# Performance work log

Measured on AMD Instinct MI355X. Metric: run time of the kernel, lower is better.

Reference implementation:

```python
import jax, jax.numpy as jnp
import numpy as np

D_MODEL = 256
N_HEADS = 8
HEAD_DIM = D_MODEL // N_HEADS


def setup_inputs() -> dict:
    key = jax.random.key(0)
    ks = jax.random.split(key, 10)
    B, L, D = 2, 2048, D_MODEL
    s = 1.0 / np.sqrt(D)
    inp = {
        "x": jax.random.normal(ks[0], (B, L, D), dtype=jnp.float32),
        "Wq": jax.random.normal(ks[1], (D, D), dtype=jnp.float32) * s,
        "bq": jnp.zeros((D,), jnp.float32),
        "Wk": jax.random.normal(ks[2], (D, D), dtype=jnp.float32) * s,
        "bk": jnp.zeros((D,), jnp.float32),
        "Wv": jax.random.normal(ks[3], (D, D), dtype=jnp.float32) * s,
        "bv": jnp.zeros((D,), jnp.float32),
        "u": jax.random.normal(ks[4], (N_HEADS, 1, 1), dtype=jnp.float32) * 0.1,
        "Wo": jax.random.normal(ks[5], (D, D), dtype=jnp.float32) * s,
        "bo": jnp.zeros((D,), jnp.float32),
    }
    return inp


def reference(x, Wq, bq, Wk, bk, Wv, bv, u, Wo, bo):
    B, L, D = x.shape
    H, hd = N_HEADS, HEAD_DIM

    def proj(W, b):  # torch Linear: x @ W.T + b -> [B,H,L,hd]
        return (x @ W.T + b).reshape(B, L, H, hd).transpose(0, 2, 1, 3)

    Q, K, V = proj(Wq, bq), proj(Wk, bk), proj(Wv, bv)

    scores = jnp.einsum("bhqd,bhkd->bhqk", Q, K) / np.sqrt(hd)
    attn_series = jax.nn.softmax(scores, axis=-1)  # [B,H,L,L]

    pos = jnp.arange(L, dtype=jnp.float32)
    dist = jnp.abs(pos[None, :] - pos[:, None])  # [L,L]
    # prior per head: exp(-d^2 / (2*(u^2+1e-6))), normalized over last dim
    prior = jnp.exp(-(dist[None] ** 2) / (2.0 * (u ** 2 + 1e-6)))  # [H,L,L]
    prior = prior / (prior.sum(axis=-1, keepdims=True) + 1e-6)

    discrepancy = jnp.abs(attn_series - prior[None]).mean(axis=(1, 2))  # [B,L]

    out = jnp.einsum("bhqk,bhkd->bhqd", attn_series, V)
    out = out.transpose(0, 2, 1, 3).reshape(B, L, D)
    out = out @ Wo.T + bo
    return out, discrepancy
```

## Files before the change

### kernel.cpp

```cpp
#include <hip/hip_runtime.h>
#include <hip/hip_bf16.h>
#include <math.h>

#define LSEQ 2048
#define DMODEL 256
#define NH 8
#define HD 32

typedef __attribute__((ext_vector_type(8))) short bf16x8;
typedef __attribute__((ext_vector_type(4))) float f32x4;

#define MFMA __builtin_amdgcn_mfma_f32_16x16x32_bf16

__device__ __forceinline__ short f2bf(float x) {
  __hip_bfloat16 h = __float2bfloat16(x);
  return __builtin_bit_cast(short, h);
}
__device__ __forceinline__ float bf2f(short s) {
  __hip_bfloat16 h = __builtin_bit_cast(__hip_bfloat16, s);
  return __bfloat162float(h);
}
__device__ __forceinline__ short bftrunc(float x) {
  return (short)(__builtin_bit_cast(unsigned int, x) >> 16);
}
__device__ __forceinline__ float fexp2(float x) {
#if __has_builtin(__builtin_amdgcn_exp2f)
  return __builtin_amdgcn_exp2f(x);
#else
  return __expf(x * 0.6931471805599453f);
#endif
}

__global__ __launch_bounds__(256) void aux_kernel(
    const float* __restrict__ x,
    const float* __restrict__ Wq, const float* __restrict__ Wk,
    const float* __restrict__ Wv, const float* __restrict__ Wo,
    const float* __restrict__ u,
    short* __restrict__ xh,
    short* __restrict__ Wh,
    short* __restrict__ Woh, short* __restrict__ Wol,
    float* __restrict__ Eb, float* __restrict__ Zb)
{
  __shared__ float Cs[LSEQ];
  __shared__ float part[256];
  const int tid = threadIdx.x;
  if (blockIdx.x < 1024) {
    const int i4 = (blockIdx.x * 256 + tid) * 4;
    float4 v = *(const float4*)(x + i4);
    *(short4*)(xh + i4) = make_short4(f2bf(v.x), f2bf(v.y), f2bf(v.z), f2bf(v.w));
    return;
  }
  const int bx = blockIdx.x - 1024;
  if (bx < 256) {
    const int i4 = (bx * 256 + tid) * 4;
    if (i4 < 196608) {
      int row = i4 >> 8, col = i4 & 255;
      const float* W = (row < 256) ? Wq : (row < 512) ? Wk : Wv;
      float4 v = *(const float4*)(W + (row & 255) * 256 + col);
      *(short4*)(Wh + i4) = make_short4(f2bf(v.x), f2bf(v.y), f2bf(v.z), f2bf(v.w));
    } else {
      int j = i4 - 196608;
      float4 v = *(const float4*)(Wo + j);
      short h0 = f2bf(v.x), h1 = f2bf(v.y), h2 = f2bf(v.z), h3 = f2bf(v.w);
      *(short4*)(Woh + j) = make_short4(h0, h1, h2, h3);
      *(short4*)(Wol + j) = make_short4(bftrunc(v.x - bf2f(h0)), bftrunc(v.y - bf2f(h1)),
                                        bftrunc(v.z - bf2f(h2)), bftrunc(v.w - bf2f(h3)));
    }
    return;
  }
  const int h = bx - 256;
  const float uu = u[h];
  const float den = 2.0f * (uu * uu + 1e-6f);
  float e[8]; float run = 0.f;
  const int base = tid * 8;
#pragma unroll
  for (int j = 0; j < 8; ++j) {
    float d = (float)(base + j);
    e[j] = __expf(-(d * d) / den);
    run += e[j];
  }
  part[tid] = run;
  __syncthreads();
  for (int off = 1; off < 256; off <<= 1) {
    float v = (tid >= off) ? part[tid - off] : 0.f;
    __syncthreads();
    part[tid] += v;
    __syncthreads();
  }
  float c = part[tid] - run;
#pragma unroll
  for (int j = 0; j < 8; ++j) {
    c += e[j];
    Cs[base + j] = c;
    Eb[h * LSEQ + base + j] = e[j];
  }
  __syncthreads();
  const float E0 = Cs[0];
  for (int i = tid; i < LSEQ; i += 256) {
    float s = Cs[i] + Cs[LSEQ - 1 - i] - E0;
    Zb[h * LSEQ + i] = 1.0f / (s + 1e-6f);
  }
}

__global__ __launch_bounds__(256) void qkv_gemm(
    const short* __restrict__ xh,
    const short* __restrict__ Bh,
    const float* __restrict__ bq, const float* __restrict__ bk,
    const float* __restrict__ bv,
    short* __restrict__ Qf, short* __restrict__ Kf, short* __restrict__ Vf)
{
  const int tid = threadIdx.x, w = tid >> 6, lane = tid & 63;
  const int l15 = lane & 15, q4 = lane >> 4;
  const int m0 = blockIdx.x * 64, n0 = blockIdx.y * 64;
  const int mrow = m0 + w * 16 + l15;
  f32x4 acc[4] = {{0,0,0,0},{0,0,0,0},{0,0,0,0},{0,0,0,0}};
  for (int k0 = 0; k0 < 256; k0 += 32) {
    bf16x8 ah = *(const bf16x8*)&xh[(size_t)mrow * 256 + k0 + q4 * 8];
#pragma unroll
    for (int nt = 0; nt < 4; ++nt) {
      const size_t bi = (size_t)(n0 + nt * 16 + l15) * 256 + k0 + q4 * 8;
      bf16x8 bh = *(const bf16x8*)&Bh[bi];
      acc[nt] = MFMA(ah, bh, acc[nt], 0, 0, 0);
    }
  }
  const int type = n0 >> 8;
  const int n0l = n0 & 255;
  const float* bias = (type == 0) ? bq : (type == 1) ? bk : bv;
  const float qls = 0.25503489f;
#pragma unroll
  for (int nt = 0; nt < 4; ++nt) {
    const int col = n0l + nt * 16 + l15;
    const float bvv = bias[col];
    const int hh = col >> 5, dloc = col & 31;
#pragma unroll
    for (int r = 0; r < 4; ++r) {
      const int m = m0 + w * 16 + q4 * 4 + r;
      float v = acc[nt][r] + bvv;
      const int bb = m >> 11, mm = m & 2047, rr = mm & 15;
      if (type == 2) {
        const int kt128 = mm >> 7, low7 = mm & 127;
        const int wv = (low7 >> 4) & 3, ph = low7 >> 6;
        const int c = ph * 16 + rr;
        const size_t idx =
          ((((((size_t)bb * 8 + hh) * 16 + kt128) * 4 + wv) * 2 + (dloc >> 4)) * 64
           + (c >> 3) * 16 + (dloc & 15)) * 8 + (c & 7);
        Vf[idx] = f2bf(v);
      } else if (type == 0) {
        const int qblk = mm >> 5, rg = (mm >> 4) & 1;
        const size_t idx =
          (((((size_t)bb * 8 + hh) * 64 + qblk) * 2 + rg) * 64
           + (dloc >> 3) * 16 + rr) * 8 + (dloc & 7);
        Qf[idx] = f2bf(v * qls);
      } else {
        const int g = mm >> 4;
        const size_t idx =
          ((((size_t)bb * 8 + hh) * 128 + g) * 64
           + (dloc >> 3) * 16 + rr) * 8 + (dloc & 7);
        Kf[idx] = f2bf(v);
      }
    }
  }
}

__global__ __launch_bounds__(512, 2) void attn_kernel(
    const short* __restrict__ Qf, const short* __restrict__ Kf,
    const short* __restrict__ Vf,
    const float* __restrict__ Eb, const float* __restrict__ Zb,
    short* __restrict__ Ohb, short* __restrict__ Olb,
    short* __restrict__ Dp)
{
  __shared__ short Pt[8][16][36];
  __shared__ float Elds[192];
  __shared__ float lpart[8][16];
  __shared__ float lpn[16];
  __shared__ float liz[16];

  const int tid = threadIdx.x, w = tid >> 6, lane = tid & 63;
  const int l15 = lane & 15, q4 = lane >> 4;
  const int flat = blockIdx.x + 128 * (blockIdx.y + 8 * blockIdx.z);
  const int slot = flat >> 3;
  const int g = (flat & 7) | ((slot >> 7) << 3);
  const int h = g & 7, b = g >> 3;
  const int qslot = slot & 127, q0 = qslot * 16;
  const int bh = b * NH + h;

  if (tid < 192) Elds[tid] = Eb[h * LSEQ + tid];
  if (tid < 16)  liz[tid] = Zb[h * LSEQ + q0 + tid];

  const bf16x8* Qf8 = (const bf16x8*)Qf;
  const bf16x8* Kf8 = (const bf16x8*)Kf;
  const bf16x8* Vf8 = (const bf16x8*)Vf;

  bf16x8 qh = Qf8[((size_t)bh * 128 + qslot) * 64 + lane];

  const size_t kfb = (size_t)bh * 128;
  const size_t vfb = (size_t)bh * 16;
  const int wv = w & 3, wh = w >> 2;

  unsigned int pc[8][4];
  float lac[4] = {0.f, 0.f, 0.f, 0.f};
  f32x4 oacc[2] = {{0,0,0,0},{0,0,0,0}};

#pragma unroll
  for (int it = 0; it < 8; ++it) {
    const int g16 = it * 16 + wh * 8 + wv;
    bf16x8 k0 = Kf8[(kfb + g16) * 64 + lane];
    bf16x8 k1 = Kf8[(kfb + g16 + 4) * 64 + lane];
    const int kt128 = it * 2 + wh;
    bf16x8 vb0 = Vf8[(((vfb + kt128) * 4 + wv) * 2 + 0) * 64 + lane];
    bf16x8 vb1 = Vf8[(((vfb + kt128) * 4 + wv) * 2 + 1) * 64 + lane];
    f32x4 s0 = {0.f,0.f,0.f,0.f}; s0 = MFMA(qh, k0, s0, 0, 0, 0);
    f32x4 s1 = {0.f,0.f,0.f,0.f}; s1 = MFMA(qh, k1, s1, 0, 0, 0);
    short c0[4], c1[4];
#pragma unroll
    for (int r = 0; r < 4; ++r) {
      float p0 = fexp2(s0[r]);
      float p1 = fexp2(s1[r]);
      lac[r] += p0 + p1;
      c0[r] = f2bf(p0);
      c1[r] = f2bf(p1);
      Pt[w][q4 * 4 + r][l15]      = c0[r];
      Pt[w][q4 * 4 + r][16 + l15] = c1[r];
    }
    pc[it][0] = (unsigned int)(unsigned short)c0[0] | ((unsigned int)(unsigned short)c0[1] << 16);
    pc[it][1] = (unsigned int)(unsigned short)c0[2] | ((unsigned int)(unsigned short)c0[3] << 16);
    pc[it][2] = (unsigned int)(unsigned short)c1[0] | ((unsigned int)(unsigned short)c1[1] << 16);
    pc[it][3] = (unsigned int)(unsigned short)c1[2] | ((unsigned int)(unsigned short)c1[3] << 16);
    bf16x8 pa = *(const bf16x8*)&Pt[w][l15][q4 * 8];
    oacc[0] = MFMA(pa, vb0, oacc[0], 0, 0, 0);
    oacc[1] = MFMA(pa, vb1, oacc[1], 0, 0, 0);
  }

#pragma unroll
  for (int r = 0; r < 4; ++r) {
    float v = lac[r];
    v += __shfl_xor(v, 1); v += __shfl_xor(v, 2);
    v += __shfl_xor(v, 4); v += __shfl_xor(v, 8);
    if (l15 == 0) lpart[w][q4 * 4 + r] = v;
  }
  __syncthreads();
  if (tid < 16) {
    float l = 0.f;
#pragma unroll
    for (int w8 = 0; w8 < 8; ++w8) l += lpart[w8][tid];
    lpn[tid] = 1.0f / l;
  }
  __syncthreads();

  float pn4[4], iz4[4];
#pragma unroll
  for (int r = 0; r < 4; ++r) {
    pn4[r] = lpn[q4 * 4 + r];
    iz4[r] = liz[q4 * 4 + r];
  }
  const int qrow0 = q0 + q4 * 4;

  const size_t drow = (size_t)(g * 128 + qslot) * LSEQ;
#pragma unroll
  for (int it = 0; it < 8; ++it) {
#pragma unroll
    for (int ph = 0; ph < 2; ++ph) {
      const int c0g = (it * 2 + wh) * 128 + ph * 64 + wv * 16;
      const int kg = c0g + l15;
      const int dd = c0g - q0;
      const bool near = (dd >= -96) && (dd <= 96);
      const unsigned int wlo = pc[it][ph * 2 + 0];
      const unsigned int whi = pc[it][ph * 2 + 1];
      float pr[4];
      pr[0] = __builtin_bit_cast(float, wlo << 16);
      pr[1] = __builtin_bit_cast(float, wlo & 0xffff0000u);
      pr[2] = __builtin_bit_cast(float, whi << 16);
      pr[3] = __builtin_bit_cast(float, whi & 0xffff0000u);
      float dsum = 0.f;
      if (near) {
#pragma unroll
        for (int r = 0; r < 4; ++r) {
          float p = pr[r] * pn4[r];
          int qrow = qrow0 + r;
          int dist = (qrow >= kg) ? (qrow - kg) : (kg - qrow);
          dsum += fabsf(p - Elds[dist] * iz4[r]);
        }
      } else {
        dsum = pr[0] * pn4[0] + pr[1] * pn4[1] + pr[2] * pn4[2] + pr[3] * pn4[3];
      }
      dsum += __shfl_xor(dsum, 16);
      dsum += __shfl_xor(dsum, 32);
      if (q4 == 0) Dp[drow + kg] = f2bf(dsum);
    }
  }

  __syncthreads();
  float* Ored = (float*)Pt;
#pragma unroll
  for (int dt = 0; dt < 2; ++dt) {
#pragma unroll
    for (int r = 0; r < 4; ++r)
      Ored[(w * 16 + q4 * 4 + r) * 17 + l15] = oacc[dt][r];
    __syncthreads();
    if (tid < 256) {
      const int q = tid >> 4, d = tid & 15;
      float v = 0.f;
#pragma unroll
      for (int w8 = 0; w8 < 8; ++w8) v += Ored[(w8 * 16 + q) * 17 + d];
      v *= lpn[q];
      const size_t oo = ((size_t)b * LSEQ + q0 + q) * DMODEL + h * HD + dt * 16 + d;
      short hi = f2bf(v);
      Ohb[oo] = hi;
      Olb[oo] = bftrunc(v - bf2f(hi));
    }
    __syncthreads();
  }
}

__global__ __launch_bounds__(256) void tail_kernel(
    const short* __restrict__ Ah, const short* __restrict__ Al,
    const short* __restrict__ Bh, const short* __restrict__ Bl,
    const float* __restrict__ bias, float* __restrict__ C,
    const short* __restrict__ Dp, float* __restrict__ disc)
{
  __shared__ float red[8][33];
  const int tid = threadIdx.x;
  if (blockIdx.x < 512) {
    const int w = tid >> 6, lane = tid & 63;
    const int l15 = lane & 15, q4 = lane >> 4;
    const int m0 = (blockIdx.x & 63) * 64, n0 = (blockIdx.x >> 6) * 32;
    const int mrow = m0 + w * 16 + l15;
    f32x4 acc[2] = {{0,0,0,0},{0,0,0,0}};
    for (int k0 = 0; k0 < 256; k0 += 32) {
      bf16x8 ah = *(const bf16x8*)&Ah[(size_t)mrow * 256 + k0 + q4 * 8];
      bf16x8 al = *(const bf16x8*)&Al[(size_t)mrow * 256 + k0 + q4 * 8];
#pragma unroll
      for (int nt = 0; nt < 2; ++nt) {
        const size_t bi = (size_t)(n0 + nt * 16 + l15) * 256 + k0 + q4 * 8;
        bf16x8 bh = *(const bf16x8*)&Bh[bi];
        bf16x8 bl = *(const bf16x8*)&Bl[bi];
        acc[nt] = MFMA(ah, bh, acc[nt], 0, 0, 0);
        acc[nt] = MFMA(al, bh, acc[nt], 0, 0, 0);
        acc[nt] = MFMA(ah, bl, acc[nt], 0, 0, 0);
      }
    }
#pragma unroll
    for (int nt = 0; nt < 2; ++nt) {
      const int col = n0 + nt * 16 + l15;
      const float bvv = bias[col];
#pragma unroll
      for (int r = 0; r < 4; ++r) {
        const int m = m0 + w * 16 + q4 * 4 + r;
        C[(size_t)m * 256 + col] = acc[nt][r] + bvv;
      }
    }
    return;
  }
  const int bid = blockIdx.x - 512;
  const int b = bid >> 6, kb = (bid & 63) * 32;
  const int k = kb + (tid & 31), sg = tid >> 5;
  float acc = 0.f;
  const short* base = Dp + ((size_t)b * 1024 + (size_t)sg * 128) * LSEQ + k;
#pragma unroll 4
  for (int i = 0; i < 128; ++i) acc += bf2f(base[(size_t)i * LSEQ]);
  red[sg][tid & 31] = acc;
  __syncthreads();
  if (tid < 32) {
    float v = 0.f;
#pragma unroll
    for (int s2 = 0; s2 < 8; ++s2) v += red[s2][tid];
    disc[b * LSEQ + kb + tid] = v * (1.0f / ((float)NH * (float)LSEQ));
  }
}

extern "C" void kernel_launch(void* const* d_in, const int* in_sizes, int n_in,
                              void* d_out, int out_size, void* d_ws, size_t ws_size,
                              hipStream_t stream)
{
  const float* x  = (const float*)d_in[0];
  const float* Wq = (const float*)d_in[1];
  const float* bq = (const float*)d_in[2];
  const float* Wk = (const float*)d_in[3];
  const float* bk = (const float*)d_in[4];
  const float* Wv = (const float*)d_in[5];
  const float* bv = (const float*)d_in[6];
  const float* u  = (const float*)d_in[7];
  const float* Wo = (const float*)d_in[8];
  const float* bo = (const float*)d_in[9];

  float* out  = (float*)d_out;
  float* disc = out + (size_t)2 * LSEQ * DMODEL;

  char* w8 = (char*)d_ws;
  const size_t MB = 1u << 20;
  short* Qfb = (short*)(w8);
  short* Kfb = (short*)(w8 + 2 * MB);
  short* Vfb = (short*)(w8 + 4 * MB);
  short* Ohb = (short*)(w8 + 6 * MB);
  short* Olb = (short*)(w8 + 8 * MB);
  short* Wh  = (short*)(w8 + 10 * MB);
  short* Woh = (short*)(w8 + 10 * MB + 393216);
  short* Wol = (short*)(w8 + 10 * MB + 524288);
  float* Eb  = (float*)(w8 + 11 * MB);
  float* Zb  = (float*)(w8 + 11 * MB + 65536);
  short* xh  = (short*)(w8 + 12 * MB);
  short* Dp  = (short*)(w8 + 14 * MB);

  aux_kernel<<<1288, 256, 0, stream>>>(x, Wq, Wk, Wv, Wo, u, xh, Wh, Woh, Wol, Eb, Zb);
  qkv_gemm<<<dim3(64, 12), 256, 0, stream>>>(xh, Wh, bq, bk, bv, Qfb, Kfb, Vfb);
  attn_kernel<<<dim3(128, 8, 2), 512, 0, stream>>>(Qfb, Kfb, Vfb, Eb, Zb,
                                                   Ohb, Olb, Dp);
  tail_kernel<<<640, 256, 0, stream>>>(Ohb, Olb, Woh, Wol, bo, out, Dp, disc);
}
```

Before: 172.7 us.

## Split attention key range across 16 waves and pack P with byte-permute truncation

The attention block grows from 512 to 1024 threads, so each of 16 waves handles 4 key tiles instead of 8, halving per-wave serial work and the register array holding packed probabilities. The bf16 conversion of probabilities switches from round-to-nearest to truncation, packed with a single v_perm, which cuts conversion ALU work but slightly changes numerics. Cross-wave reductions now sum 16 partials, and the launch bound asks for 8 blocks per CU, which may force heavy register limiting and extra shared memory per block.

```diff
diff --git a/kernel.cpp b/kernel.cpp
--- a/kernel.cpp
+++ b/kernel.cpp
@@ -29,6 +29,11 @@
 #else
   return __expf(x * 0.6931471805599453f);
 #endif
+}
+__device__ __forceinline__ unsigned int packtrunc(float lo, float hi) {
+  return __builtin_amdgcn_perm(__builtin_bit_cast(unsigned int, hi),
+                               __builtin_bit_cast(unsigned int, lo),
+                               0x07060302u);
 }
 
 __global__ __launch_bounds__(256) void aux_kernel(
@@ -162,16 +167,16 @@
   }
 }
 
-__global__ __launch_bounds__(512, 2) void attn_kernel(
+__global__ __launch_bounds__(1024, 8) void attn_kernel(
     const short* __restrict__ Qf, const short* __restrict__ Kf,
     const short* __restrict__ Vf,
     const float* __restrict__ Eb, const float* __restrict__ Zb,
     short* __restrict__ Ohb, short* __restrict__ Olb,
     short* __restrict__ Dp)
 {
-  __shared__ short Pt[8][16][36];
+  __shared__ short Pt[16][16][36];
   __shared__ float Elds[192];
-  __shared__ float lpart[8][16];
+  __shared__ float lpart[16][16];
   __shared__ float lpn[16];
   __shared__ float liz[16];
 
@@ -195,37 +200,35 @@
 
   const size_t kfb = (size_t)bh * 128;
   const size_t vfb = (size_t)bh * 16;
-  const int wv = w & 3, wh = w >> 2;
-
-  unsigned int pc[8][4];
+  const int wv = w & 3, wq = w >> 2;
+
+  unsigned int pc[4][4];
   float lac[4] = {0.f, 0.f, 0.f, 0.f};
   f32x4 oacc[2] = {{0,0,0,0},{0,0,0,0}};
 
 #pragma unroll
-  for (int it = 0; it < 8; ++it) {
-    const int g16 = it * 16 + wh * 8 + wv;
-    bf16x8 k0 = Kf8[(kfb + g16) * 64 + lane];
-    bf16x8 k1 = Kf8[(kfb + g16 + 4) * 64 + lane];
-    const int kt128 = it * 2 + wh;
+  for (int it = 0; it < 4; ++it) {
+    const int kt128 = wq + 4 * it;
+    const int gk = kt128 * 8 + wv;
+    bf16x8 k0 = Kf8[(kfb + gk) * 64 + lane];
+    bf16x8 k1 = Kf8[(kfb + gk + 4) * 64 + lane];
     bf16x8 vb0 = Vf8[(((vfb + kt128) * 4 + wv) * 2 + 0) * 64 + lane];
     bf16x8 vb1 = Vf8[(((vfb + kt128) * 4 + wv) * 2 + 1) * 64 + lane];
     f32x4 s0 = {0.f,0.f,0.f,0.f}; s0 = MFMA(qh, k0, s0, 0, 0, 0);
     f32x4 s1 = {0.f,0.f,0.f,0.f}; s1 = MFMA(qh, k1, s1, 0, 0, 0);
-    short c0[4], c1[4];
+    float p0[4], p1[4];
 #pragma unroll
     for (int r = 0; r < 4; ++r) {
-      float p0 = fexp2(s0[r]);
-      float p1 = fexp2(s1[r]);
-      lac[r] += p0 + p1;
-      c0[r] = f2bf(p0);
-      c1[r] = f2bf(p1);
-      Pt[w][q4 * 4 + r][l15]      = c0[r];
-      Pt[w][q4 * 4 + r][16 + l15] = c1[r];
-    }
-    pc[it][0] = (unsigned int)(unsigned short)c0[0] | ((unsigned int)(unsigned short)c0[1] << 16);
-    pc[it][1] = (unsigned int)(unsigned short)c0[2] | ((unsigned int)(unsigned short)c0[3] << 16);
-    pc[it][2] = (unsigned int)(unsigned short)c1[0] | ((unsigned int)(unsigned short)c1[1] << 16);
-    pc[it][3] = (unsigned int)(unsigned short)c1[2] | ((unsigned int)(unsigned short)c1[3] << 16);
+      p0[r] = fexp2(s0[r]);
+      p1[r] = fexp2(s1[r]);
+      lac[r] += p0[r] + p1[r];
+      Pt[w][q4 * 4 + r][l15]      = bftrunc(p0[r]);
+      Pt[w][q4 * 4 + r][16 + l15] = bftrunc(p1[r]);
+    }
+    pc[it][0] = packtrunc(p0[0], p0[1]);
+    pc[it][1] = packtrunc(p0[2], p0[3]);
+    pc[it][2] = packtrunc(p1[0], p1[1]);
+    pc[it][3] = packtrunc(p1[2], p1[3]);
     bf16x8 pa = *(const bf16x8*)&Pt[w][l15][q4 * 8];
     oacc[0] = MFMA(pa, vb0, oacc[0], 0, 0, 0);
     oacc[1] = MFMA(pa, vb1, oacc[1], 0, 0, 0);
@@ -242,7 +245,7 @@
   if (tid < 16) {
     float l = 0.f;
 #pragma unroll
-    for (int w8 = 0; w8 < 8; ++w8) l += lpart[w8][tid];
+    for (int w16 = 0; w16 < 16; ++w16) l += lpart[w16][tid];
     lpn[tid] = 1.0f / l;
   }
   __syncthreads();
@@ -257,10 +260,11 @@
 
   const size_t drow = (size_t)(g * 128 + qslot) * LSEQ;
 #pragma unroll
-  for (int it = 0; it < 8; ++it) {
+  for (int it = 0; it < 4; ++it) {
+    const int kt128 = wq + 4 * it;
 #pragma unroll
     for (int ph = 0; ph < 2; ++ph) {
-      const int c0g = (it * 2 + wh) * 128 + ph * 64 + wv * 16;
+      const int c0g = kt128 * 128 + ph * 64 + wv * 16;
       const int kg = c0g + l15;
       const int dd = c0g - q0;
       const bool near = (dd >= -96) && (dd <= 96);
@@ -301,7 +305,7 @@
       const int q = tid >> 4, d = tid & 15;
       float v = 0.f;
 #pragma unroll
-      for (int w8 = 0; w8 < 8; ++w8) v += Ored[(w8 * 16 + q) * 17 + d];
+      for (int w16 = 0; w16 < 16; ++w16) v += Ored[(w16 * 16 + q) * 17 + d];
       v *= lpn[q];
       const size_t oo = ((size_t)b * LSEQ + q0 + q) * DMODEL + h * HD + dt * 16 + d;
       short hi = f2bf(v);
@@ -403,7 +407,7 @@
 
   aux_kernel<<<1288, 256, 0, stream>>>(x, Wq, Wk, Wv, Wo, u, xh, Wh, Woh, Wol, Eb, Zb);
   qkv_gemm<<<dim3(64, 12), 256, 0, stream>>>(xh, Wh, bq, bk, bv, Qfb, Kfb, Vfb);
-  attn_kernel<<<dim3(128, 8, 2), 512, 0, stream>>>(Qfb, Kfb, Vfb, Eb, Zb,
-                                                   Ohb, Olb, Dp);
+  attn_kernel<<<dim3(128, 8, 2), 1024, 0, stream>>>(Qfb, Kfb, Vfb, Eb, Zb,
+                                                    Ohb, Olb, Dp);
   tail_kernel<<<640, 256, 0, stream>>>(Ohb, Olb, Woh, Wol, bo, out, Dp, disc);
 }
```

Measured after the change: 157.4 us. 8.9% less time.
